# Kernel tuning notes

Measured on AMD Instinct MI355X. Metric: run time of the kernel, lower is better.

The kernel has to match this reference:

```python
import jax, jax.numpy as jnp
import numpy as np

D_MODEL = 1024
NUM_HEADS = 16
HEAD_DIM = D_MODEL // NUM_HEADS


def setup_inputs() -> dict:
    key = jax.random.key(0)
    k_x, k_qkv, k_proj, k_pb = jax.random.split(key, 4)
    x = jax.random.normal(k_x, (4, 2048, D_MODEL), dtype=jnp.float32)
    s = 1.0 / np.sqrt(D_MODEL)
    W_qkv = jax.random.uniform(k_qkv, (D_MODEL, 3 * D_MODEL), minval=-s, maxval=s, dtype=jnp.float32)
    W_proj = jax.random.uniform(k_proj, (D_MODEL, D_MODEL), minval=-s, maxval=s, dtype=jnp.float32)
    b_proj = jax.random.uniform(k_pb, (D_MODEL,), minval=-s, maxval=s, dtype=jnp.float32)
    return {"x": x, "W_qkv": W_qkv, "W_proj": W_proj, "b_proj": b_proj}


def reference(x, W_qkv, W_proj, b_proj):
    B, N, D = x.shape
    H, Hd = NUM_HEADS, HEAD_DIM
    scale = Hd ** -0.5
    qkv = jnp.einsum('bnd,de->bne', x, W_qkv)  # (B, N, 3D), no bias (qkv_bias=False)
    qkv = qkv.reshape(B, N, 3, H, Hd).transpose(2, 0, 3, 1, 4)  # (3, B, H, N, Hd)
    q, k, v = qkv[0], qkv[1], qkv[2]
    attn = jnp.einsum('bhqd,bhkd->bhqk', q, k) * scale  # (B, H, N, N)
    attn = jax.nn.softmax(attn, axis=-1)
    out = jnp.einsum('bhqk,bhkd->bhqd', attn, v)  # (B, H, N, Hd)
    out = out.transpose(0, 2, 1, 3).reshape(B, N, D)
    return jnp.einsum('bnd,de->bne', out, W_proj) + b_proj
```

## Files before the change

### kernel.cpp

```cpp
#include <hip/hip_runtime.h>


#define DEV __device__ __forceinline__

typedef __attribute__((ext_vector_type(8))) short bf16x8;
typedef __attribute__((ext_vector_type(4))) float f32x4;
typedef __attribute__((ext_vector_type(2))) __bf16 bf16x2v;

DEV unsigned short f2b(float f) {
  union { float f; unsigned u; } x; x.f = f;
  unsigned r = (x.u + 0x7FFFu + ((x.u >> 16) & 1u)) >> 16;
  return (unsigned short)r;
}

DEV unsigned pkbf(float a, float b) {
  bf16x2v v; v[0] = (__bf16)a; v[1] = (__bf16)b;
  union { bf16x2v v; unsigned u; } x; x.v = v; return x.u;
}

#if __has_builtin(__builtin_amdgcn_exp2f)
DEV float fexp2(float x) { return __builtin_amdgcn_exp2f(x); }
#else
DEV float fexp2(float x) { return __exp2f(x); }
#endif

DEV void gload16(const void* g, void* l) {
  __builtin_amdgcn_global_load_lds((const __attribute__((address_space(1))) void*)g,
                                   (__attribute__((address_space(3))) void*)l,
                                   16, 0, 0);
}

__global__ void k_cvt(const float* __restrict__ in, unsigned short* __restrict__ out) {
  int i = (blockIdx.x * 256 + threadIdx.x) * 4;
  float4 v = *(const float4*)&in[i];
  *(uint2*)&out[i] = make_uint2(pkbf(v.x, v.y), pkbf(v.z, v.w));
}

__global__ void k_wt(const float* __restrict__ W, unsigned short* __restrict__ Wt,
                     int Nw, int K) {
  __shared__ float t[64][65];
  const int k0 = blockIdx.y * 64, n0 = blockIdx.x * 64;
  const int tx = threadIdx.x, ty = threadIdx.y;
#pragma unroll
  for (int i = 0; i < 16; ++i) {
    int r = i * 4 + ty;
    t[r][tx] = W[(size_t)(k0 + r) * Nw + n0 + tx];
  }
  __syncthreads();
#pragma unroll
  for (int i = 0; i < 16; ++i) {
    int r = i * 4 + ty;
    Wt[(size_t)(n0 + r) * K + k0 + tx] = f2b(t[tx][r]);
  }
}

__global__ void k_vt(const unsigned short* __restrict__ qkv, unsigned short* __restrict__ vt) {
  __shared__ unsigned short t[64][68];
  const int bh = blockIdx.y;
  const int b = bh >> 4, h = bh & 15;
  const int n0 = blockIdx.x * 64;
  const int tx = threadIdx.x, ty = threadIdx.y;
#pragma unroll
  for (int i = 0; i < 16; ++i) {
    int r = i * 4 + ty;
    t[r][tx] = qkv[(size_t)(b * 2048 + n0 + r) * 3072 + 2048 + h * 64 + tx];
  }
  __syncthreads();
#pragma unroll
  for (int i = 0; i < 16; ++i) {
    int d = i * 4 + ty;
    vt[(size_t)(bh * 64 + d) * 2048 + n0 + tx] = t[tx][d];
  }
}

template <bool PROJ>
__global__ __launch_bounds__(256, 2) void gemm_bt(
    const unsigned short* __restrict__ A, const unsigned short* __restrict__ Bt,
    unsigned short* __restrict__ outB, float* __restrict__ outF,
    const float* __restrict__ bias, int M, int N, int K) {
  __shared__ unsigned short Al[2][128 * 32];
  __shared__ unsigned short Bl[2][128 * 32];
  const int tid = threadIdx.x;
  const int lane = tid & 63;
  const int wv = tid >> 6;
  const int m0 = blockIdx.y * 128;
  const int n0 = blockIdx.x * 128;
  const int wrow = (wv >> 1) * 64;
  const int wcol = (wv & 1) * 64;

  f32x4 acc[4][4];
#pragma unroll
  for (int i = 0; i < 4; ++i)
#pragma unroll
    for (int j = 0; j < 4; ++j) acc[i][j] = (f32x4){0.f, 0.f, 0.f, 0.f};

  const int lr = lane >> 2;
  const int lk = (lane & 3) * 8;
  const int fr = lane & 15;
  const int fg = (lane >> 4) * 8;

  const unsigned short* gA = A + (size_t)(m0 + wv * 32 + lr) * K + lk;
  const unsigned short* gB = Bt + (size_t)(n0 + wv * 32 + lr) * K + lk;

  auto STAGE = [&](int buf, int kt) {
    const size_t k0 = (size_t)kt << 5;
    unsigned short* a = &Al[buf][(wv * 2) * 512];
    unsigned short* b = &Bl[buf][(wv * 2) * 512];
    gload16(gA + k0, a);
    gload16(gA + k0 + (size_t)16 * K, a + 512);
    gload16(gB + k0, b);
    gload16(gB + k0 + (size_t)16 * K, b + 512);
  };

  const int nk = K >> 5;
  STAGE(0, 0);
  for (int kt = 0; kt < nk; ++kt) {
    const int cur = kt & 1;
    __syncthreads();
    if (kt + 1 < nk) STAGE(cur ^ 1, kt + 1);
    const unsigned short* Ab = &Al[cur][0];
    const unsigned short* Bb = &Bl[cur][0];
    bf16x8 af[4], bfv[4];
#pragma unroll
    for (int i = 0; i < 4; ++i) af[i] = *(const bf16x8*)&Ab[(wrow + i * 16 + fr) * 32 + fg];
#pragma unroll
    for (int j = 0; j < 4; ++j) bfv[j] = *(const bf16x8*)&Bb[(wcol + j * 16 + fr) * 32 + fg];
    __builtin_amdgcn_s_setprio(1);
#pragma unroll
    for (int i = 0; i < 4; ++i)
#pragma unroll
      for (int j = 0; j < 4; ++j)
        acc[i][j] = __builtin_amdgcn_mfma_f32_16x16x32_bf16(af[i], bfv[j], acc[i][j], 0, 0, 0);
    __builtin_amdgcn_s_setprio(0);
  }

  const int rg = (lane >> 4) * 4;
#pragma unroll
  for (int i = 0; i < 4; ++i) {
#pragma unroll
    for (int j = 0; j < 4; ++j) {
      const int col = n0 + wcol + j * 16 + fr;
#pragma unroll
      for (int r = 0; r < 4; ++r) {
        const int row = m0 + wrow + i * 16 + rg + r;
        if (PROJ)
          outF[(size_t)row * N + col] = acc[i][j][r] + bias[col];
        else
          outB[(size_t)row * N + col] = f2b(acc[i][j][r]);
      }
    }
  }
}

__global__ __launch_bounds__(256, 3) void attn_k(
    const unsigned short* __restrict__ qkv, const unsigned short* __restrict__ vt,
    unsigned short* __restrict__ ao) {
  __shared__ unsigned short Kl[2][64 * 64];
  __shared__ unsigned short Vl[2][64 * 64];
  __shared__ unsigned short Pl[4][32 * 72];
  const int tid = threadIdx.x;
  const int lane = tid & 63;
  const int wv = tid >> 6;
  const int id = blockIdx.x;
  const int swz = (id & 7) * (1024 >> 3) + (id >> 3);
  const int bh = swz >> 4;
  const int b = bh >> 4, h = bh & 15;
  const int q0 = (swz & 15) * 128 + wv * 32;
  const int fr = lane & 15;
  const int hi = lane >> 4;
  const int g8 = hi * 8;
  const int g4 = hi * 4;
  const int fx = fr & 7;
  const float CSC = 0.125f * 1.44269504f;
  const float THR = 4.0f;

  const int sr = lane >> 3;
  const int sc = ((lane & 7) ^ (sr & 7)) * 8;
  const unsigned short* gK =
      qkv + (size_t)(b * 2048 + wv * 16 + sr) * 3072 + 1024 + h * 64 + sc;
  const unsigned short* gV =
      vt + ((size_t)bh * 64 + wv * 16 + sr) * 2048 + sc;

  bf16x8 bq[2][2];
#pragma unroll
  for (int qt = 0; qt < 2; ++qt)
#pragma unroll
    for (int ks = 0; ks < 2; ++ks)
      bq[qt][ks] = *(const bf16x8*)&qkv[(size_t)(b * 2048 + q0 + qt * 16 + fr) * 3072 +
                                        h * 64 + ks * 32 + g8];

  bf16x8 vones;
#pragma unroll
  for (int j = 0; j < 8; ++j) vones[j] = (short)0x3F80;

  f32x4 acc[4][2];
  f32x4 acc_l[2];
#pragma unroll
  for (int i = 0; i < 4; ++i)
#pragma unroll
    for (int j = 0; j < 2; ++j) acc[i][j] = (f32x4){0.f, 0.f, 0.f, 0.f};
  acc_l[0] = (f32x4){0.f, 0.f, 0.f, 0.f};
  acc_l[1] = (f32x4){0.f, 0.f, 0.f, 0.f};
  float m[2] = {-1e30f, -1e30f};

  auto STAGE = [&](int buf, int tt) {
#pragma unroll
    for (int seg = 0; seg < 2; ++seg) {
      gload16(gK + (size_t)(tt * 64 + seg * 8) * 3072, &Kl[buf][(wv * 16 + seg * 8) * 64]);
      gload16(gV + (size_t)(seg * 8) * 2048 + tt * 64, &Vl[buf][(wv * 16 + seg * 8) * 64]);
    }
  };

  int cur = 0;
  STAGE(0, 0);
  __syncthreads();

  const f32x4 csc4 = (f32x4){CSC, CSC, CSC, CSC};

  for (int tt = 0; tt < 32; ++tt) {
    if (tt < 31) STAGE(cur ^ 1, tt + 1);
    const unsigned short* Kb = &Kl[cur][0];
    const unsigned short* Vb = &Vl[cur][0];

    f32x4 st[4][2];
    __builtin_amdgcn_s_setprio(1);
#pragma unroll
    for (int kk = 0; kk < 4; ++kk) {
      bf16x8 ak0 = *(const bf16x8*)&Kb[(kk * 16 + fr) * 64 + ((hi ^ fx) * 8)];
      bf16x8 ak1 = *(const bf16x8*)&Kb[(kk * 16 + fr) * 64 + (((4 + hi) ^ fx) * 8)];
#pragma unroll
      for (int qt = 0; qt < 2; ++qt) {
        f32x4 z = (f32x4){0.f, 0.f, 0.f, 0.f};
        z = __builtin_amdgcn_mfma_f32_16x16x32_bf16(ak0, bq[qt][0], z, 0, 0, 0);
        st[kk][qt] = __builtin_amdgcn_mfma_f32_16x16x32_bf16(ak1, bq[qt][1], z, 0, 0, 0);
      }
    }
    __builtin_amdgcn_s_setprio(0);

    f32x4 t0 = __builtin_elementwise_max(st[0][0], st[1][0]);
    t0 = __builtin_elementwise_max(t0, st[2][0]);
    t0 = __builtin_elementwise_max(t0, st[3][0]);
    f32x4 t1 = __builtin_elementwise_max(st[0][1], st[1][1]);
    t1 = __builtin_elementwise_max(t1, st[2][1]);
    t1 = __builtin_elementwise_max(t1, st[3][1]);
    const float c0 = fmaxf(fmaxf(t0[0], t0[1]), fmaxf(t0[2], t0[3])) * CSC;
    const float c1 = fmaxf(fmaxf(t1[0], t1[1]), fmaxf(t1[2], t1[3])) * CSC;

    if (!__all(c0 <= m[0] + THR && c1 <= m[1] + THR)) {
      const float cc[2] = {c0, c1};
#pragma unroll
      for (int qt = 0; qt < 2; ++qt) {
        float tm = cc[qt];
        tm = fmaxf(tm, __shfl_xor(tm, 16, 64));
        tm = fmaxf(tm, __shfl_xor(tm, 32, 64));
        const float mnew = fmaxf(m[qt], tm);
        const float corr = fexp2(m[qt] - mnew);
        m[qt] = mnew;
        acc_l[qt][0] *= corr;
#pragma unroll
        for (int dt = 0; dt < 4; ++dt) acc[dt][qt] *= corr;
      }
    }

#pragma unroll
    for (int qt = 0; qt < 2; ++qt) {
      const float mq = m[qt];
      const f32x4 mq4 = (f32x4){-mq, -mq, -mq, -mq};
      const int prow = (qt * 16 + fr) * 72;
#pragma unroll
      for (int kk = 0; kk < 4; ++kk) {
        f32x4 e = __builtin_elementwise_fma(st[kk][qt], csc4, mq4);
        *(uint2*)&Pl[wv][prow + kk * 16 + g4] =
            make_uint2(pkbf(fexp2(e[0]), fexp2(e[1])), pkbf(fexp2(e[2]), fexp2(e[3])));
      }
    }

#pragma unroll
    for (int ks2 = 0; ks2 < 2; ++ks2) {
      bf16x8 bp0 = *(const bf16x8*)&Pl[wv][(0 * 16 + fr) * 72 + ks2 * 32 + g8];
      bf16x8 bp1 = *(const bf16x8*)&Pl[wv][(1 * 16 + fr) * 72 + ks2 * 32 + g8];
      __builtin_amdgcn_s_setprio(1);
#pragma unroll
      for (int dt = 0; dt < 4; ++dt) {
        bf16x8 av = *(const bf16x8*)&Vb[(dt * 16 + fr) * 64 + (((ks2 * 4 + hi) ^ fx) * 8)];
        acc[dt][0] = __builtin_amdgcn_mfma_f32_16x16x32_bf16(av, bp0, acc[dt][0], 0, 0, 0);
        acc[dt][1] = __builtin_amdgcn_mfma_f32_16x16x32_bf16(av, bp1, acc[dt][1], 0, 0, 0);
      }
      acc_l[0] = __builtin_amdgcn_mfma_f32_16x16x32_bf16(vones, bp0, acc_l[0], 0, 0, 0);
      acc_l[1] = __builtin_amdgcn_mfma_f32_16x16x32_bf16(vones, bp1, acc_l[1], 0, 0, 0);
      __builtin_amdgcn_s_setprio(0);
    }

    __syncthreads();
    cur ^= 1;
  }

#pragma unroll
  for (int qt = 0; qt < 2; ++qt) {
    const float inv = 1.0f / acc_l[qt][0];
#pragma unroll
    for (int dt = 0; dt < 4; ++dt) {
      uint2 o = make_uint2(pkbf(acc[dt][qt][0] * inv, acc[dt][qt][1] * inv),
                           pkbf(acc[dt][qt][2] * inv, acc[dt][qt][3] * inv));
      *(uint2*)&ao[(size_t)(b * 2048 + q0 + qt * 16 + fr) * 1024 + h * 64 + dt * 16 + g4] = o;
    }
  }
}

extern "C" void kernel_launch(void* const* d_in, const int* in_sizes, int n_in,
                              void* d_out, int out_size, void* d_ws, size_t ws_size,
                              hipStream_t stream) {
  const float* x     = (const float*)d_in[0];
  const float* wqkv  = (const float*)d_in[1];
  const float* wproj = (const float*)d_in[2];
  const float* bproj = (const float*)d_in[3];
  float* out = (float*)d_out;
  char* ws = (char*)d_ws;

  unsigned short* xb     = (unsigned short*)(ws + 0);
  unsigned short* wqkvT  = (unsigned short*)(ws + 16777216);
  unsigned short* wprojT = (unsigned short*)(ws + 23068672);
  unsigned short* qkv    = (unsigned short*)(ws + 25165824);
  unsigned short* vt     = (unsigned short*)(ws + 75497472);
  unsigned short* ao     = (unsigned short*)(ws + 92274688);

  k_cvt<<<8192, 256, 0, stream>>>(x, xb);
  k_wt<<<dim3(48, 16), dim3(64, 4), 0, stream>>>(wqkv, wqkvT, 3072, 1024);
  k_wt<<<dim3(16, 16), dim3(64, 4), 0, stream>>>(wproj, wprojT, 1024, 1024);
  gemm_bt<false><<<dim3(24, 64), 256, 0, stream>>>(xb, wqkvT, qkv, nullptr, nullptr,
                                                   8192, 3072, 1024);
  k_vt<<<dim3(32, 64), dim3(64, 4), 0, stream>>>(qkv, vt);
  attn_k<<<1024, 256, 0, stream>>>(qkv, vt, ao);
  gemm_bt<true><<<dim3(8, 64), 256, 0, stream>>>(ao, wprojT, nullptr, out, bproj,
                                                 8192, 1024, 1024);
}
```

Measured before the change: 295.0 us.

## Double attention query tile per block to reuse staged K/V tiles

Each attention block now handles 256 query rows (64 per wave) instead of 128, processing two 32-row sub-tiles against each staged K/V tile, and the grid shrinks from 1024 to 512 blocks. This halves the number of times each K/V tile is loaded from global memory into LDS per query, spreading the staging and barrier costs over more work. In exchange it needs more registers for accumulators and Q fragments, lowers the launch-bounds occupancy hint from 3 to 2 blocks, and gives fewer blocks to cover the CUs.

```diff
diff --git a/kernel.cpp b/kernel.cpp
--- a/kernel.cpp
+++ b/kernel.cpp
@@ -152,7 +152,7 @@
   }
 }
 
-__global__ __launch_bounds__(256, 3) void attn_k(
+__global__ __launch_bounds__(256, 2) void attn_k(
     const unsigned short* __restrict__ qkv, const unsigned short* __restrict__ vt,
     unsigned short* __restrict__ ao) {
   __shared__ unsigned short Kl[2][64 * 64];
@@ -162,10 +162,10 @@
   const int lane = tid & 63;
   const int wv = tid >> 6;
   const int id = blockIdx.x;
-  const int swz = (id & 7) * (1024 >> 3) + (id >> 3);
-  const int bh = swz >> 4;
+  const int swz = (id & 7) * 64 + (id >> 3);
+  const int bh = swz >> 3;
   const int b = bh >> 4, h = bh & 15;
-  const int q0 = (swz & 15) * 128 + wv * 32;
+  const int q0 = (swz & 7) * 256 + wv * 64;
   const int fr = lane & 15;
   const int hi = lane >> 4;
   const int g8 = hi * 8;
@@ -181,9 +181,9 @@
   const unsigned short* gV =
       vt + ((size_t)bh * 64 + wv * 16 + sr) * 2048 + sc;
 
-  bf16x8 bq[2][2];
-#pragma unroll
-  for (int qt = 0; qt < 2; ++qt)
+  bf16x8 bq[4][2];
+#pragma unroll
+  for (int qt = 0; qt < 4; ++qt)
 #pragma unroll
     for (int ks = 0; ks < 2; ++ks)
       bq[qt][ks] = *(const bf16x8*)&qkv[(size_t)(b * 2048 + q0 + qt * 16 + fr) * 3072 +
@@ -193,15 +193,15 @@
 #pragma unroll
   for (int j = 0; j < 8; ++j) vones[j] = (short)0x3F80;
 
-  f32x4 acc[4][2];
-  f32x4 acc_l[2];
+  f32x4 acc[4][4];
+  f32x4 acc_l[4];
 #pragma unroll
   for (int i = 0; i < 4; ++i)
 #pragma unroll
-    for (int j = 0; j < 2; ++j) acc[i][j] = (f32x4){0.f, 0.f, 0.f, 0.f};
-  acc_l[0] = (f32x4){0.f, 0.f, 0.f, 0.f};
-  acc_l[1] = (f32x4){0.f, 0.f, 0.f, 0.f};
-  float m[2] = {-1e30f, -1e30f};
+    for (int j = 0; j < 4; ++j) acc[i][j] = (f32x4){0.f, 0.f, 0.f, 0.f};
+#pragma unroll
+  for (int j = 0; j < 4; ++j) acc_l[j] = (f32x4){0.f, 0.f, 0.f, 0.f};
+  float m[4] = {-1e30f, -1e30f, -1e30f, -1e30f};
 
   auto STAGE = [&](int buf, int tt) {
 #pragma unroll
@@ -222,73 +222,79 @@
     const unsigned short* Kb = &Kl[cur][0];
     const unsigned short* Vb = &Vl[cur][0];
 
-    f32x4 st[4][2];
-    __builtin_amdgcn_s_setprio(1);
-#pragma unroll
-    for (int kk = 0; kk < 4; ++kk) {
-      bf16x8 ak0 = *(const bf16x8*)&Kb[(kk * 16 + fr) * 64 + ((hi ^ fx) * 8)];
-      bf16x8 ak1 = *(const bf16x8*)&Kb[(kk * 16 + fr) * 64 + (((4 + hi) ^ fx) * 8)];
-#pragma unroll
-      for (int qt = 0; qt < 2; ++qt) {
-        f32x4 z = (f32x4){0.f, 0.f, 0.f, 0.f};
-        z = __builtin_amdgcn_mfma_f32_16x16x32_bf16(ak0, bq[qt][0], z, 0, 0, 0);
-        st[kk][qt] = __builtin_amdgcn_mfma_f32_16x16x32_bf16(ak1, bq[qt][1], z, 0, 0, 0);
-      }
-    }
-    __builtin_amdgcn_s_setprio(0);
-
-    f32x4 t0 = __builtin_elementwise_max(st[0][0], st[1][0]);
-    t0 = __builtin_elementwise_max(t0, st[2][0]);
-    t0 = __builtin_elementwise_max(t0, st[3][0]);
-    f32x4 t1 = __builtin_elementwise_max(st[0][1], st[1][1]);
-    t1 = __builtin_elementwise_max(t1, st[2][1]);
-    t1 = __builtin_elementwise_max(t1, st[3][1]);
-    const float c0 = fmaxf(fmaxf(t0[0], t0[1]), fmaxf(t0[2], t0[3])) * CSC;
-    const float c1 = fmaxf(fmaxf(t1[0], t1[1]), fmaxf(t1[2], t1[3])) * CSC;
-
-    if (!__all(c0 <= m[0] + THR && c1 <= m[1] + THR)) {
-      const float cc[2] = {c0, c1};
-#pragma unroll
-      for (int qt = 0; qt < 2; ++qt) {
-        float tm = cc[qt];
-        tm = fmaxf(tm, __shfl_xor(tm, 16, 64));
-        tm = fmaxf(tm, __shfl_xor(tm, 32, 64));
-        const float mnew = fmaxf(m[qt], tm);
-        const float corr = fexp2(m[qt] - mnew);
-        m[qt] = mnew;
-        acc_l[qt][0] *= corr;
-#pragma unroll
-        for (int dt = 0; dt < 4; ++dt) acc[dt][qt] *= corr;
-      }
-    }
-
-#pragma unroll
-    for (int qt = 0; qt < 2; ++qt) {
-      const float mq = m[qt];
-      const f32x4 mq4 = (f32x4){-mq, -mq, -mq, -mq};
-      const int prow = (qt * 16 + fr) * 72;
+#pragma unroll
+    for (int qtb = 0; qtb < 2; ++qtb) {
+      const int qA = qtb * 2, qB = qtb * 2 + 1;
+
+      f32x4 st[4][2];
+      __builtin_amdgcn_s_setprio(1);
 #pragma unroll
       for (int kk = 0; kk < 4; ++kk) {
-        f32x4 e = __builtin_elementwise_fma(st[kk][qt], csc4, mq4);
-        *(uint2*)&Pl[wv][prow + kk * 16 + g4] =
-            make_uint2(pkbf(fexp2(e[0]), fexp2(e[1])), pkbf(fexp2(e[2]), fexp2(e[3])));
-      }
-    }
-
-#pragma unroll
-    for (int ks2 = 0; ks2 < 2; ++ks2) {
-      bf16x8 bp0 = *(const bf16x8*)&Pl[wv][(0 * 16 + fr) * 72 + ks2 * 32 + g8];
-      bf16x8 bp1 = *(const bf16x8*)&Pl[wv][(1 * 16 + fr) * 72 + ks2 * 32 + g8];
-      __builtin_amdgcn_s_setprio(1);
-#pragma unroll
-      for (int dt = 0; dt < 4; ++dt) {
-        bf16x8 av = *(const bf16x8*)&Vb[(dt * 16 + fr) * 64 + (((ks2 * 4 + hi) ^ fx) * 8)];
-        acc[dt][0] = __builtin_amdgcn_mfma_f32_16x16x32_bf16(av, bp0, acc[dt][0], 0, 0, 0);
-        acc[dt][1] = __builtin_amdgcn_mfma_f32_16x16x32_bf16(av, bp1, acc[dt][1], 0, 0, 0);
-      }
-      acc_l[0] = __builtin_amdgcn_mfma_f32_16x16x32_bf16(vones, bp0, acc_l[0], 0, 0, 0);
-      acc_l[1] = __builtin_amdgcn_mfma_f32_16x16x32_bf16(vones, bp1, acc_l[1], 0, 0, 0);
+        bf16x8 ak0 = *(const bf16x8*)&Kb[(kk * 16 + fr) * 64 + ((hi ^ fx) * 8)];
+        bf16x8 ak1 = *(const bf16x8*)&Kb[(kk * 16 + fr) * 64 + (((4 + hi) ^ fx) * 8)];
+#pragma unroll
+        for (int j = 0; j < 2; ++j) {
+          f32x4 z = (f32x4){0.f, 0.f, 0.f, 0.f};
+          z = __builtin_amdgcn_mfma_f32_16x16x32_bf16(ak0, bq[qA + j][0], z, 0, 0, 0);
+          st[kk][j] = __builtin_amdgcn_mfma_f32_16x16x32_bf16(ak1, bq[qA + j][1], z, 0, 0, 0);
+        }
+      }
       __builtin_amdgcn_s_setprio(0);
+
+      f32x4 t0 = __builtin_elementwise_max(st[0][0], st[1][0]);
+      t0 = __builtin_elementwise_max(t0, st[2][0]);
+      t0 = __builtin_elementwise_max(t0, st[3][0]);
+      f32x4 t1 = __builtin_elementwise_max(st[0][1], st[1][1]);
+      t1 = __builtin_elementwise_max(t1, st[2][1]);
+      t1 = __builtin_elementwise_max(t1, st[3][1]);
+      const float c0 = fmaxf(fmaxf(t0[0], t0[1]), fmaxf(t0[2], t0[3])) * CSC;
+      const float c1 = fmaxf(fmaxf(t1[0], t1[1]), fmaxf(t1[2], t1[3])) * CSC;
+
+      if (!__all(c0 <= m[qA] + THR && c1 <= m[qB] + THR)) {
+        const float cc[2] = {c0, c1};
+#pragma unroll
+        for (int j = 0; j < 2; ++j) {
+          const int qt = qA + j;
+          float tm = cc[j];
+          tm = fmaxf(tm, __shfl_xor(tm, 16, 64));
+          tm = fmaxf(tm, __shfl_xor(tm, 32, 64));
+          const float mnew = fmaxf(m[qt], tm);
+          const float corr = fexp2(m[qt] - mnew);
+          m[qt] = mnew;
+          acc_l[qt][0] *= corr;
+#pragma unroll
+          for (int dt = 0; dt < 4; ++dt) acc[dt][qt] *= corr;
+        }
+      }
+
+#pragma unroll
+      for (int j = 0; j < 2; ++j) {
+        const float mq = m[qA + j];
+        const f32x4 mq4 = (f32x4){-mq, -mq, -mq, -mq};
+        const int prow = (j * 16 + fr) * 72;
+#pragma unroll
+        for (int kk = 0; kk < 4; ++kk) {
+          f32x4 e = __builtin_elementwise_fma(st[kk][j], csc4, mq4);
+          *(uint2*)&Pl[wv][prow + kk * 16 + g4] =
+              make_uint2(pkbf(fexp2(e[0]), fexp2(e[1])), pkbf(fexp2(e[2]), fexp2(e[3])));
+        }
+      }
+
+#pragma unroll
+      for (int ks2 = 0; ks2 < 2; ++ks2) {
+        bf16x8 bp0 = *(const bf16x8*)&Pl[wv][(0 * 16 + fr) * 72 + ks2 * 32 + g8];
+        bf16x8 bp1 = *(const bf16x8*)&Pl[wv][(1 * 16 + fr) * 72 + ks2 * 32 + g8];
+        __builtin_amdgcn_s_setprio(1);
+#pragma unroll
+        for (int dt = 0; dt < 4; ++dt) {
+          bf16x8 av = *(const bf16x8*)&Vb[(dt * 16 + fr) * 64 + (((ks2 * 4 + hi) ^ fx) * 8)];
+          acc[dt][qA] = __builtin_amdgcn_mfma_f32_16x16x32_bf16(av, bp0, acc[dt][qA], 0, 0, 0);
+          acc[dt][qB] = __builtin_amdgcn_mfma_f32_16x16x32_bf16(av, bp1, acc[dt][qB], 0, 0, 0);
+        }
+        acc_l[qA] = __builtin_amdgcn_mfma_f32_16x16x32_bf16(vones, bp0, acc_l[qA], 0, 0, 0);
+        acc_l[qB] = __builtin_amdgcn_mfma_f32_16x16x32_bf16(vones, bp1, acc_l[qB], 0, 0, 0);
+        __builtin_amdgcn_s_setprio(0);
+      }
     }
 
     __syncthreads();
@@ -296,7 +302,7 @@
   }
 
 #pragma unroll
-  for (int qt = 0; qt < 2; ++qt) {
+  for (int qt = 0; qt < 4; ++qt) {
     const float inv = 1.0f / acc_l[qt][0];
 #pragma unroll
     for (int dt = 0; dt < 4; ++dt) {
@@ -330,7 +336,7 @@
   gemm_bt<false><<<dim3(24, 64), 256, 0, stream>>>(xb, wqkvT, qkv, nullptr, nullptr,
                                                    8192, 3072, 1024);
   k_vt<<<dim3(32, 64), dim3(64, 4), 0, stream>>>(qkv, vt);
-  attn_k<<<1024, 256, 0, stream>>>(qkv, vt, ao);
+  attn_k<<<512, 256, 0, stream>>>(qkv, vt, ao);
   gemm_bt<true><<<dim3(8, 64), 256, 0, stream>>>(ao, wprojT, nullptr, out, bproj,
                                                  8192, 1024, 1024);
 }
```

Result: faster. 288.3 us (-2.3%).
